# Optimization experiments

Hardware: AMD Instinct MI355X
Metric: run time of the kernel (lower is better)

## Reference

```python
import jax, jax.numpy as jnp
import numpy as np

B, T, D, L, E = 8, 2048, 256, 8, 64


def setup_inputs() -> dict:
    key = jax.random.key(0)
    ks = jax.random.split(key, 5)
    x = jax.random.normal(ks[0], (B, T, D), dtype=jnp.float32)
    # MMLP params: weight (4L, D, E), bias (4L, E); nn.Linear: (2L, D), (2L,)
    W_ml = jax.random.normal(ks[1], (4 * L, D, E), dtype=jnp.float32) * 0.05
    b_ml = jax.random.normal(ks[2], (4 * L, E), dtype=jnp.float32) * 0.05
    W_lin = jax.random.normal(ks[3], (2 * L, D), dtype=jnp.float32) * 0.05
    b_lin = jax.random.normal(ks[4], (2 * L,), dtype=jnp.float32) * 0.05
    return {"x": x, "W_ml": W_ml, "b_ml": b_ml, "W_lin": W_lin, "b_lin": b_lin}


def _xlstm_forward(x, W_ml, b_ml, W_lin, b_lin):
    b, t, _ = x.shape
    l4, _, e = W_ml.shape
    l = l4 // 4
    # Precompute all per-step gate projections at once (the torch code does this per step).
    mg = jnp.einsum('bti,lij->btlj', x, W_ml) + b_ml          # (B,T,4L,E)
    lg = jnp.einsum('bti,li->btl', x, W_lin) + b_lin          # (B,T,2L)
    o_, v, k, q = jnp.split(mg, 4, axis=2)                    # each (B,T,L,E)
    i_, f_ = jnp.split(lg, 2, axis=2)                         # each (B,T,L)
    xs = tuple(jnp.moveaxis(a, 1, 0) for a in (o_, v, k, q, i_, f_))  # time-major

    def step(carry, inp):
        m, n, C, h = carry
        o_t, v_t, k_t, q_t, i_t, f_t = inp
        m_new = jnp.maximum(f_t + m, i_t)                     # stabilizer (B,L)
        i_g = jnp.exp(i_t - m_new)
        f_g = jnp.exp(f_t + m - m_new)
        # rank-1 outer-product update of matrix cell state (B,L,E,E)
        C = f_g[:, :, None, None] * C + i_g[:, :, None, None] * (v_t[:, :, :, None] * k_t[:, :, None, :])
        n = f_g[:, :, None] * n + i_g[:, :, None] * k_t       # (B,L,E)
        denom = jnp.maximum(jnp.sum(n * q_t, axis=-1), 1.0)[:, :, None]  # clamp(.,1,inf)
        h = jax.nn.sigmoid(o_t) * jnp.einsum('blij,bli->blj', C, q_t) / denom
        return (m_new, n, C, h), None

    init = (
        jnp.zeros((b, l), jnp.float32),
        jnp.zeros((b, l, e), jnp.float32),
        jnp.zeros((b, l, e, e), jnp.float32),
        jnp.zeros((b, l, e), jnp.float32),
    )
    (m, n, C, h), _ = jax.lax.scan(step, init, xs)
    return h, C


def reference(x, W_ml, b_ml, W_lin, b_lin):
    return _xlstm_forward(x, W_ml, b_ml, W_lin, b_lin)
```

## Files before the change

### kernel.cpp

```cpp
#include <hip/hip_runtime.h>

#define B 8
#define T 2048
#define D 256
#define L 8
#define E 64
#define BT (B*T)

typedef _Float16 f16;
typedef f16 f16x8 __attribute__((ext_vector_type(8)));
typedef float f32x4 __attribute__((ext_vector_type(4)));

#define OFF_I   0
#define OFF_F   (OFF_I  + B*L*T)
#define OFF_WT  (OFF_F  + B*L*T)
#define OFF_VT  (OFF_WT + 16*E*D/2)
#define OFF_KT  (OFF_VT + B*L*E*T/2)
#define OFF_CP  (OFF_KT + B*L*E*T/2)
#define OFF_X16 (OFF_CP + 64*4*4160)

__global__ __launch_bounds__(256) void k_prep_all(const float* __restrict__ x,
        const float* __restrict__ Wlin, const float* __restrict__ blin,
        const float* __restrict__ Wml,
        float* __restrict__ ibuf, float* __restrict__ fbuf,
        f16* __restrict__ Wt16, f16* __restrict__ x16) {
    __shared__ __align__(16) char smem[49920];
    int tid = threadIdx.x;
    int bx = blockIdx.x;
    if (bx < 512) {
        float (*xs)[260] = (float(*)[260])smem;
        float (*wsm)[260] = (float(*)[260])(smem + 33280);
        int t0 = bx * 32;
        {
            int row = tid >> 3, q = tid & 7;
            const float* src = x + (size_t)(t0 + row) * D + q * 32;
            #pragma unroll
            for (int j = 0; j < 8; ++j) {
                float4 v = *(const float4*)(src + j * 4);
                *(float4*)&xs[row][q * 32 + j * 4] = v;
            }
        }
        {
            int row = tid >> 4, c0 = (tid & 15) * 16;
            const float* src = Wlin + row * D + c0;
            #pragma unroll
            for (int j = 0; j < 4; ++j) {
                float4 v = *(const float4*)(src + j * 4);
                *(float4*)&wsm[row][c0 + j * 4] = v;
            }
        }
        __syncthreads();
        int tl = tid >> 4, g = tid & 15;
        float acc0 = 0.f, acc1 = 0.f;
        for (int i = 0; i < D; ++i) {
            float wv = wsm[g][i];
            acc0 += xs[tl * 2 + 0][i] * wv;
            acc1 += xs[tl * 2 + 1][i] * wv;
        }
        float bias = blin[g];
        float acc[2] = {acc0 + bias, acc1 + bias};
        #pragma unroll
        for (int u = 0; u < 2; ++u) {
            int t = t0 + tl * 2 + u;
            int b = t >> 11, tt = t & 2047;
            if (g < 8) ibuf[(b * L + g) * T + tt] = acc[u];
            else       fbuf[(b * L + (g - 8)) * T + tt] = acc[u];
        }
    } else if (bx < 528) {
        float (*ts)[65] = (float(*)[65])smem;
        int vkrow = bx - 512;
        int wrow = 8 + vkrow;
        for (int dc = 0; dc < 4; ++dc) {
            int d0 = dc * 64;
            int r = tid >> 2, cq = (tid & 3) * 16;
            const float* src = Wml + ((size_t)wrow * D + d0 + r) * E + cq;
            #pragma unroll
            for (int j = 0; j < 16; j += 4) {
                float4 v = *(const float4*)(src + j);
                ts[r][cq + j] = v.x; ts[r][cq + j + 1] = v.y;
                ts[r][cq + j + 2] = v.z; ts[r][cq + j + 3] = v.w;
            }
            __syncthreads();
            int e = tid >> 2, dq = (tid & 3) * 16;
            f16* dst = Wt16 + ((size_t)vkrow * E + e) * D + d0 + dq;
            f16x8 o0, o1;
            #pragma unroll
            for (int j = 0; j < 8; ++j) {
                o0[j] = (f16)ts[dq + j][e];
                o1[j] = (f16)ts[dq + 8 + j][e];
            }
            *(f16x8*)dst = o0;
            *(f16x8*)(dst + 8) = o1;
            __syncthreads();
        }
    } else {
        int i = ((bx - 528) * 256 + tid) * 8;
        float4 v0 = *(const float4*)(x + i);
        float4 v1 = *(const float4*)(x + i + 4);
        f16x8 o;
        o[0] = (f16)v0.x; o[1] = (f16)v0.y; o[2] = (f16)v0.z; o[3] = (f16)v0.w;
        o[4] = (f16)v1.x; o[5] = (f16)v1.y; o[6] = (f16)v1.z; o[7] = (f16)v1.w;
        *(f16x8*)(x16 + i) = o;
    }
}

__global__ __launch_bounds__(512) void k_vkproj3(const f16* __restrict__ x16,
        const f16* __restrict__ Wt16, const float* __restrict__ bml,
        f16* __restrict__ Vt, f16* __restrict__ Kt) {
    __shared__ __align__(16) char lds[40960];
    int tid = threadIdx.x;
    int bx = blockIdx.x, h = blockIdx.y;
    int t0 = bx * 128;
    const f16* xa = x16 + (size_t)t0 * D;
    const f16* wb = Wt16 + (size_t)h * 8 * E * D;
    int wv = tid >> 6, lane = tid & 63;
    int wr = wv >> 2, wc = wv & 3;
    int q = lane >> 4, lr = lane & 15;
    int sa_t = tid >> 2, sa_q = tid & 3;
    f32x4 acc[4][8] = {};
    for (int ks = 0; ks < 8; ++ks) {
        int k0 = ks * 32;
        {
            f16x8 v = *(const f16x8*)(xa + (size_t)sa_t * D + k0 + sa_q * 8);
            int ba = sa_t * 64 + ((sa_q ^ ((sa_t >> 1) & 3)) << 4);
            *(f16x8*)(lds + ba) = v;
        }
        #pragma unroll
        for (int rr = 0; rr < 4; ++rr) {
            int r = rr * 128 + (tid >> 2);
            int c = tid & 3;
            f16x8 v = *(const f16x8*)(wb + (size_t)r * D + k0 + c * 8);
            int ba = 8192 + r * 64 + ((c ^ ((r >> 1) & 3)) << 4);
            *(f16x8*)(lds + ba) = v;
        }
        __syncthreads();
        f16x8 a[4], bf[8];
        #pragma unroll
        for (int m = 0; m < 4; ++m) {
            int t = wr * 64 + m * 16 + lr;
            int ba = t * 64 + ((q ^ ((t >> 1) & 3)) << 4);
            a[m] = *(const f16x8*)(lds + ba);
        }
        #pragma unroll
        for (int n = 0; n < 8; ++n) {
            int c = wc * 128 + n * 16 + lr;
            int ba = 8192 + c * 64 + ((q ^ ((c >> 1) & 3)) << 4);
            bf[n] = *(const f16x8*)(lds + ba);
        }
        #pragma unroll
        for (int m = 0; m < 4; ++m)
            #pragma unroll
            for (int n = 0; n < 8; ++n)
                acc[m][n] = __builtin_amdgcn_mfma_f32_16x16x32_f16(
                    a[m], bf[n], acc[m][n], 0, 0, 0);
        __syncthreads();
    }
    const float* bp = bml + (size_t)(8 + h * 8) * E;
    int b_g = t0 >> 11, tin = t0 & 2047;
    f16* obase = h ? Kt : Vt;
    for (int p = 0; p < 4; ++p) {
        if (wc == p) {
            #pragma unroll
            for (int n = 0; n < 8; ++n) {
                int cc = n * 16 + lr;
                float bias = bp[p * 128 + cc];
                int swz = (cc & 7) << 4;
                #pragma unroll
                for (int m = 0; m < 4; ++m) {
                    #pragma unroll
                    for (int r = 0; r < 4; r += 2) {
                        int t = wr * 64 + m * 16 + q * 4 + r;
                        union { f16 h2[2]; unsigned u; } pk;
                        pk.h2[0] = (f16)(acc[m][n][r] + bias);
                        pk.h2[1] = (f16)(acc[m][n][r + 1] + bias);
                        int ba = cc * 256 + ((t * 2) ^ swz);
                        *(unsigned*)(lds + ba) = pk.u;
                    }
                }
            }
        }
        __syncthreads();
        {
            int cc = tid >> 2, part = tid & 3;
            int cg = p * 128 + cc;
            int l = cg >> 6, e = cg & 63;
            f16* dst = obase + ((size_t)((b_g * L + l) * E + e)) * T + tin + part * 32;
            int swz = (cc & 7) << 4;
            #pragma unroll
            for (int jj = 0; jj < 4; ++jj) {
                int t = part * 32 + jj * 8;
                int ba = cc * 256 + ((t * 2) ^ swz);
                *(f16x8*)(dst + jj * 8) = *(const f16x8*)(lds + ba);
            }
        }
        __syncthreads();
    }
}

__global__ __launch_bounds__(256) void k_cgemm2s(const f16* __restrict__ Vt,
        const f16* __restrict__ Kt, const float* __restrict__ ibuf,
        const float* __restrict__ fbuf, float* __restrict__ Cpart) {
    __shared__ float red[64 * 64];
    __shared__ float redn[64];
    __shared__ float part[256];
    __shared__ float rmax[256];
    __shared__ __align__(16) f16 wlds[512];
    int tid = threadIdx.x;
    int bl = blockIdx.x, tc = blockIdx.y;
    int wv = tid >> 6, lane = tid & 63;
    {
        const float* fp = fbuf + bl * T + tid * 8;
        const float* ip = ibuf + bl * T + tid * 8;
        float4 fa = *(const float4*)fp;
        float4 fb = *(const float4*)(fp + 4);
        float4 ia = *(const float4*)ip;
        float4 ib = *(const float4*)(ip + 4);
        float f[8] = {fa.x, fa.y, fa.z, fa.w, fb.x, fb.y, fb.z, fb.w};
        float iv[8] = {ia.x, ia.y, ia.z, ia.w, ib.x, ib.y, ib.z, ib.w};
        float ls[8]; float run = 0.f;
        #pragma unroll
        for (int r = 0; r < 8; ++r) { run += f[r]; ls[r] = run; }
        part[tid] = run;
        __syncthreads();
        float inc = run;
        #pragma unroll
        for (int s = 1; s < 256; s <<= 1) {
            float u = (tid >= s) ? part[tid - s] : 0.f;
            __syncthreads();
            inc += u;
            part[tid] = inc;
            __syncthreads();
        }
        float off = inc - run;
        float e[8]; float lmax = -1e30f;
        #pragma unroll
        for (int r = 0; r < 8; ++r) { e[r] = iv[r] - (off + ls[r]); lmax = fmaxf(lmax, e[r]); }
        rmax[tid] = lmax;
        __syncthreads();
        for (int s = 128; s > 0; s >>= 1) {
            if (tid < s) rmax[tid] = fmaxf(rmax[tid], rmax[tid + s]);
            __syncthreads();
        }
        float M = fmaxf(rmax[0], 0.0f);
        int t = tid * 8;
        if ((t >> 9) == tc) {
            f16x8 w8;
            #pragma unroll
            for (int r = 0; r < 8; ++r) w8[r] = (f16)__expf(e[r] - M);
            *(f16x8*)&wlds[t & 511] = w8;
        }
        __syncthreads();
    }
    const f16* vp = Vt + (size_t)bl * E * T;
    const f16* kp = Kt + (size_t)bl * E * T;
    f32x4 acc[5][4] = {};
    int tbase = tc * 512 + wv * 128;
    for (int kc = 0; kc < 4; ++kc) {
        int tt = tbase + kc * 32 + (lane >> 4) * 8;
        f16x8 wfrag = *(const f16x8*)&wlds[tt & 511];
        f16x8 a[5], bf[4];
        #pragma unroll
        for (int m = 0; m < 4; ++m) {
            int i = m * 16 + (lane & 15);
            f16x8 v = *(const f16x8*)(vp + (size_t)i * T + tt);
            a[m] = v * wfrag;
        }
        a[4] = wfrag;
        #pragma unroll
        for (int nn = 0; nn < 4; ++nn) {
            int j = nn * 16 + (lane & 15);
            bf[nn] = *(const f16x8*)(kp + (size_t)j * T + tt);
        }
        #pragma unroll
        for (int m = 0; m < 5; ++m)
            #pragma unroll
            for (int nn = 0; nn < 4; ++nn)
                acc[m][nn] = __builtin_amdgcn_mfma_f32_16x16x32_f16(
                    a[m], bf[nn], acc[m][nn], 0, 0, 0);
    }
    for (int rr = 0; rr < 4; ++rr) {
        if (wv == rr) {
            #pragma unroll
            for (int m = 0; m < 4; ++m)
                #pragma unroll
                for (int nn = 0; nn < 4; ++nn)
                    #pragma unroll
                    for (int r = 0; r < 4; ++r) {
                        int row = m * 16 + (lane >> 4) * 4 + r;
                        int col = nn * 16 + (lane & 15);
                        if (rr == 0) red[row * 64 + col] = acc[m][nn][r];
                        else         red[row * 64 + col] += acc[m][nn][r];
                    }
            if ((lane >> 4) == 0) {
                #pragma unroll
                for (int nn = 0; nn < 4; ++nn) {
                    int col = nn * 16 + (lane & 15);
                    if (rr == 0) redn[col] = acc[4][nn][0];
                    else         redn[col] += acc[4][nn][0];
                }
            }
        }
        __syncthreads();
    }
    float* cp = Cpart + ((size_t)bl * 4 + tc) * 4160;
    #pragma unroll
    for (int j = 0; j < 4; ++j) {
        int idx = tid * 16 + j * 4;
        *(float4*)(cp + idx) = *(const float4*)(red + idx);
    }
    if (tid < 64) cp[4096 + tid] = redn[tid];
}

__global__ __launch_bounds__(256) void k_final(const float* __restrict__ x,
        const float* __restrict__ Wml, const float* __restrict__ bml,
        const float* __restrict__ Cpart, float* __restrict__ out) {
    __shared__ float Cs[E * E];
    __shared__ float xs[D];
    __shared__ float ns[E];
    __shared__ float os[E];
    __shared__ float qs[E];
    int tid = threadIdx.x;
    int bl = blockIdx.x; int b = bl >> 3, l = bl & 7;
    xs[tid] = x[((size_t)(b * T + (T - 1))) * D + tid];
    const float* cp = Cpart + (size_t)bl * 4 * 4160;
    #pragma unroll
    for (int j = 0; j < 4; ++j) {
        int idx = tid * 16 + j * 4;
        float4 s = {0, 0, 0, 0};
        #pragma unroll
        for (int p = 0; p < 4; ++p) {
            float4 v = *(const float4*)(cp + p * 4160 + idx);
            s.x += v.x; s.y += v.y; s.z += v.z; s.w += v.w;
        }
        *(float4*)&Cs[idx] = s;
        *(float4*)(out + 4096 + (size_t)bl * (E * E) + idx) = s;
    }
    if (tid < 64) {
        float s = 0.f;
        #pragma unroll
        for (int p = 0; p < 4; ++p) s += cp[p * 4160 + 4096 + tid];
        ns[tid] = s;
    }
    __syncthreads();
    if (tid < 128) {
        int gate = tid >> 6, e = tid & 63;
        int wrow = gate ? (3 * L + l) : l;
        const float* wpp = Wml + (size_t)wrow * D * E + e;
        float s = 0.f;
        for (int kk = 0; kk < D; ++kk) s += xs[kk] * wpp[kk * E];
        s += bml[wrow * E + e];
        if (gate) qs[e] = s; else os[e] = s;
    }
    __syncthreads();
    if (tid < 64) {
        int j = tid;
        float hc = 0.f;
        for (int i2 = 0; i2 < E; ++i2) hc += Cs[i2 * E + j] * qs[i2];
        float nq = 0.f;
        for (int i2 = 0; i2 < E; ++i2) nq += ns[i2] * qs[i2];
        float denom = fmaxf(nq, 1.0f);
        float sg = 1.0f / (1.0f + __expf(-os[j]));
        out[bl * E + j] = sg * hc / denom;
    }
}

extern "C" void kernel_launch(void* const* d_in, const int* in_sizes, int n_in,
                              void* d_out, int out_size, void* d_ws, size_t ws_size,
                              hipStream_t stream) {
    const float* x    = (const float*)d_in[0];
    const float* Wml  = (const float*)d_in[1];
    const float* bml  = (const float*)d_in[2];
    const float* Wlin = (const float*)d_in[3];
    const float* blin = (const float*)d_in[4];
    float* out = (float*)d_out;
    float* ws = (float*)d_ws;
    float* ibuf  = ws + OFF_I;
    float* fbuf  = ws + OFF_F;
    f16*   Wt16  = (f16*)(ws + OFF_WT);
    f16*   Vt    = (f16*)(ws + OFF_VT);
    f16*   Kt    = (f16*)(ws + OFF_KT);
    float* Cpart = ws + OFF_CP;
    f16*   x16   = (f16*)(ws + OFF_X16);

    k_prep_all<<<2576, 256, 0, stream>>>(x, Wlin, blin, Wml, ibuf, fbuf, Wt16, x16);
    k_vkproj3<<<dim3(BT / 128, 2), 512, 0, stream>>>(x16, Wt16, bml, Vt, Kt);
    k_cgemm2s<<<dim3(B * L, 4), 256, 0, stream>>>(Vt, Kt, ibuf, fbuf, Cpart);
    k_final<<<B * L, 256, 0, stream>>>(x, Wml, bml, Cpart, out);
}
```

Baseline: 65.34 us.

## Fuse final reduction into cgemm via atomic counter, use direct global-to-LDS loads

Measured after the change: 107.8 us. 1.65x slower.

```diff
diff --git a/kernel.cpp b/kernel.cpp
--- a/kernel.cpp
+++ b/kernel.cpp
@@ -16,14 +16,17 @@
 #define OFF_WT  (OFF_F  + B*L*T)
 #define OFF_VT  (OFF_WT + 16*E*D/2)
 #define OFF_KT  (OFF_VT + B*L*E*T/2)
-#define OFF_CP  (OFF_KT + B*L*E*T/2)
-#define OFF_X16 (OFF_CP + 64*4*4160)
-
-__global__ __launch_bounds__(256) void k_prep_all(const float* __restrict__ x,
+#define OFF_X16 (OFF_KT + B*L*E*T/2)
+#define OFF_OQ  (OFF_X16 + BT*D/2)
+#define OFF_CP  (OFF_OQ + 64*128)
+#define OFF_CNT (OFF_CP + 64*4*4160)
+
+__global__ __launch_bounds__(256) void k_prep(const float* __restrict__ x,
         const float* __restrict__ Wlin, const float* __restrict__ blin,
-        const float* __restrict__ Wml,
+        const float* __restrict__ Wml, const float* __restrict__ bml,
         float* __restrict__ ibuf, float* __restrict__ fbuf,
-        f16* __restrict__ Wt16, f16* __restrict__ x16) {
+        f16* __restrict__ Wt16, f16* __restrict__ x16,
+        float* __restrict__ oqbuf, unsigned int* __restrict__ cnt) {
     __shared__ __align__(16) char smem[49920];
     int tid = threadIdx.x;
     int bx = blockIdx.x;
@@ -93,7 +96,7 @@
             *(f16x8*)(dst + 8) = o1;
             __syncthreads();
         }
-    } else {
+    } else if (bx < 2576) {
         int i = ((bx - 528) * 256 + tid) * 8;
         float4 v0 = *(const float4*)(x + i);
         float4 v1 = *(const float4*)(x + i + 4);
@@ -101,6 +104,30 @@
         o[0] = (f16)v0.x; o[1] = (f16)v0.y; o[2] = (f16)v0.z; o[3] = (f16)v0.w;
         o[4] = (f16)v1.x; o[5] = (f16)v1.y; o[6] = (f16)v1.z; o[7] = (f16)v1.w;
         *(f16x8*)(x16 + i) = o;
+    } else if (bx < 2584) {
+        float (*x8)[256] = (float(*)[256])smem;
+        int l = bx - 2576;
+        {
+            int bb = tid >> 5, c = (tid & 31) * 8;
+            const float* src = x + ((size_t)(bb * T + (T - 1))) * D + c;
+            float4 v0 = *(const float4*)src, v1 = *(const float4*)(src + 4);
+            *(float4*)&x8[bb][c] = v0;
+            *(float4*)&x8[bb][c + 4] = v1;
+        }
+        __syncthreads();
+        #pragma unroll
+        for (int r = 0; r < 4; ++r) {
+            int idx = r * 256 + tid;
+            int gate = idx >> 9, b = (idx >> 6) & 7, e = idx & 63;
+            int row = gate ? (24 + l) : l;
+            const float* gp = Wml + (size_t)row * D * E + e;
+            float s = 0.f;
+            for (int kk = 0; kk < D; ++kk) s += x8[b][kk] * gp[(size_t)kk * E];
+            s += bml[row * E + e];
+            oqbuf[(b * L + l) * 128 + gate * 64 + e] = s;
+        }
+    } else {
+        if (tid < 64) cnt[tid] = 0u;
     }
 }
 
@@ -116,23 +143,30 @@
     int wv = tid >> 6, lane = tid & 63;
     int wr = wv >> 2, wc = wv & 3;
     int q = lane >> 4, lr = lane & 15;
-    int sa_t = tid >> 2, sa_q = tid & 3;
+    int srow_a = (wv << 4) + (lane >> 2);
+    int schk = lane & 3;
+    int sca = ((schk ^ ((srow_a >> 1) & 3)) << 3);
     f32x4 acc[4][8] = {};
     for (int ks = 0; ks < 8; ++ks) {
         int k0 = ks * 32;
         {
-            f16x8 v = *(const f16x8*)(xa + (size_t)sa_t * D + k0 + sa_q * 8);
-            int ba = sa_t * 64 + ((sa_q ^ ((sa_t >> 1) & 3)) << 4);
-            *(f16x8*)(lds + ba) = v;
+            const f16* src = xa + (size_t)srow_a * D + k0 + sca;
+            __builtin_amdgcn_global_load_lds(
+                (const __attribute__((address_space(1))) unsigned int*)src,
+                (__attribute__((address_space(3))) unsigned int*)(lds + (wv << 10)),
+                16, 0, 0);
         }
         #pragma unroll
         for (int rr = 0; rr < 4; ++rr) {
-            int r = rr * 128 + (tid >> 2);
-            int c = tid & 3;
-            f16x8 v = *(const f16x8*)(wb + (size_t)r * D + k0 + c * 8);
-            int ba = 8192 + r * 64 + ((c ^ ((r >> 1) & 3)) << 4);
-            *(f16x8*)(lds + ba) = v;
-        }
+            int r = rr * 128 + (wv << 4) + (lane >> 2);
+            int co = ((schk ^ ((r >> 1) & 3)) << 3);
+            const f16* src = wb + (size_t)r * D + k0 + co;
+            __builtin_amdgcn_global_load_lds(
+                (const __attribute__((address_space(1))) unsigned int*)src,
+                (__attribute__((address_space(3))) unsigned int*)(lds + 8192 + rr * 8192 + (wv << 10)),
+                16, 0, 0);
+        }
+        asm volatile("s_waitcnt vmcnt(0)" ::: "memory");
         __syncthreads();
         f16x8 a[4], bf[8];
         #pragma unroll
@@ -182,8 +216,8 @@
         __syncthreads();
         {
             int cc = tid >> 2, part = tid & 3;
-            int cg = p * 128 + cc;
-            int l = cg >> 6, e = cg & 63;
+            int cg2 = p * 128 + cc;
+            int l = cg2 >> 6, e = cg2 & 63;
             f16* dst = obase + ((size_t)((b_g * L + l) * E + e)) * T + tin + part * 32;
             int swz = (cc & 7) << 4;
             #pragma unroll
@@ -197,14 +231,18 @@
     }
 }
 
-__global__ __launch_bounds__(256) void k_cgemm2s(const f16* __restrict__ Vt,
+__global__ __launch_bounds__(256) void k_cgemm_fused(const f16* __restrict__ Vt,
         const f16* __restrict__ Kt, const float* __restrict__ ibuf,
-        const float* __restrict__ fbuf, float* __restrict__ Cpart) {
-    __shared__ float red[64 * 64];
-    __shared__ float redn[64];
-    __shared__ float part[256];
-    __shared__ float rmax[256];
-    __shared__ __align__(16) f16 wlds[512];
+        const float* __restrict__ fbuf, const float* __restrict__ oqbuf,
+        float* __restrict__ Cpart, unsigned int* __restrict__ cnt,
+        float* __restrict__ out) {
+    __shared__ __align__(16) char smem[18816];
+    float* red  = (float*)smem;
+    float* redn = (float*)(smem + 16384);
+    float* wtot = (float*)(smem + 16640);
+    float* wmax = (float*)(smem + 16656);
+    f16*   wlds = (f16*)(smem + 16672);
+    int*   flag = (int*)(smem + 17696);
     int tid = threadIdx.x;
     int bl = blockIdx.x, tc = blockIdx.y;
     int wv = tid >> 6, lane = tid & 63;
@@ -215,39 +253,37 @@
         float4 fb = *(const float4*)(fp + 4);
         float4 ia = *(const float4*)ip;
         float4 ib = *(const float4*)(ip + 4);
-        float f[8] = {fa.x, fa.y, fa.z, fa.w, fb.x, fb.y, fb.z, fb.w};
+        float f0[8] = {fa.x, fa.y, fa.z, fa.w, fb.x, fb.y, fb.z, fb.w};
         float iv[8] = {ia.x, ia.y, ia.z, ia.w, ib.x, ib.y, ib.z, ib.w};
         float ls[8]; float run = 0.f;
         #pragma unroll
-        for (int r = 0; r < 8; ++r) { run += f[r]; ls[r] = run; }
-        part[tid] = run;
-        __syncthreads();
-        float inc = run;
-        #pragma unroll
-        for (int s = 1; s < 256; s <<= 1) {
-            float u = (tid >= s) ? part[tid - s] : 0.f;
-            __syncthreads();
-            inc += u;
-            part[tid] = inc;
-            __syncthreads();
-        }
-        float off = inc - run;
+        for (int r = 0; r < 8; ++r) { run += f0[r]; ls[r] = run; }
+        float sc = run;
+        #pragma unroll
+        for (int s = 1; s < 64; s <<= 1) {
+            float u = __shfl_up(sc, s, 64);
+            if (lane >= s) sc += u;
+        }
+        if (lane == 63) wtot[wv] = sc;
+        __syncthreads();
+        float woff = 0.f;
+        #pragma unroll
+        for (int w2 = 0; w2 < 4; ++w2) if (w2 < wv) woff += wtot[w2];
+        float off = woff + sc - run;
         float e[8]; float lmax = -1e30f;
         #pragma unroll
         for (int r = 0; r < 8; ++r) { e[r] = iv[r] - (off + ls[r]); lmax = fmaxf(lmax, e[r]); }
-        rmax[tid] = lmax;
-        __syncthreads();
-        for (int s = 128; s > 0; s >>= 1) {
-            if (tid < s) rmax[tid] = fmaxf(rmax[tid], rmax[tid + s]);
-            __syncthreads();
-        }
-        float M = fmaxf(rmax[0], 0.0f);
-        int t = tid * 8;
-        if ((t >> 9) == tc) {
+        #pragma unroll
+        for (int s = 1; s < 64; s <<= 1) lmax = fmaxf(lmax, __shfl_xor(lmax, s, 64));
+        if (lane == 0) wmax[wv] = lmax;
+        __syncthreads();
+        float M = fmaxf(fmaxf(fmaxf(wmax[0], wmax[1]), fmaxf(wmax[2], wmax[3])), 0.f);
+        int tg = tid * 8;
+        if ((tg >> 9) == tc) {
             f16x8 w8;
             #pragma unroll
             for (int r = 0; r < 8; ++r) w8[r] = (f16)__expf(e[r] - M);
-            *(f16x8*)&wlds[t & 511] = w8;
+            *(f16x8*)&wlds[tg & 511] = w8;
         }
         __syncthreads();
     }
@@ -255,9 +291,11 @@
     const f16* kp = Kt + (size_t)bl * E * T;
     f32x4 acc[5][4] = {};
     int tbase = tc * 512 + wv * 128;
+    #pragma unroll
     for (int kc = 0; kc < 4; ++kc) {
-        int tt = tbase + kc * 32 + (lane >> 4) * 8;
-        f16x8 wfrag = *(const f16x8*)&wlds[tt & 511];
+        int lo = wv * 128 + kc * 32 + (lane >> 4) * 8;
+        int tt = tc * 512 + lo;
+        f16x8 wfrag = *(const f16x8*)&wlds[lo];
         f16x8 a[5], bf[4];
         #pragma unroll
         for (int m = 0; m < 4; ++m) {
@@ -278,6 +316,7 @@
                 acc[m][nn] = __builtin_amdgcn_mfma_f32_16x16x32_f16(
                     a[m], bf[nn], acc[m][nn], 0, 0, 0);
     }
+    (void)tbase;
     for (int rr = 0; rr < 4; ++rr) {
         if (wv == rr) {
             #pragma unroll
@@ -309,58 +348,46 @@
         *(float4*)(cp + idx) = *(const float4*)(red + idx);
     }
     if (tid < 64) cp[4096 + tid] = redn[tid];
-}
-
-__global__ __launch_bounds__(256) void k_final(const float* __restrict__ x,
-        const float* __restrict__ Wml, const float* __restrict__ bml,
-        const float* __restrict__ Cpart, float* __restrict__ out) {
-    __shared__ float Cs[E * E];
-    __shared__ float xs[D];
-    __shared__ float ns[E];
-    __shared__ float os[E];
-    __shared__ float qs[E];
-    int tid = threadIdx.x;
-    int bl = blockIdx.x; int b = bl >> 3, l = bl & 7;
-    xs[tid] = x[((size_t)(b * T + (T - 1))) * D + tid];
-    const float* cp = Cpart + (size_t)bl * 4 * 4160;
+    __threadfence();
+    if (tid == 0) {
+        unsigned old = atomicAdd(&cnt[bl], 1u);
+        *flag = (old == 3u);
+    }
+    __syncthreads();
+    if (!*flag) return;
+    __threadfence();
+    const float* cpb = Cpart + (size_t)bl * 4 * 4160;
     #pragma unroll
     for (int j = 0; j < 4; ++j) {
         int idx = tid * 16 + j * 4;
         float4 s = {0, 0, 0, 0};
         #pragma unroll
         for (int p = 0; p < 4; ++p) {
-            float4 v = *(const float4*)(cp + p * 4160 + idx);
+            float4 v = *(const float4*)(cpb + p * 4160 + idx);
             s.x += v.x; s.y += v.y; s.z += v.z; s.w += v.w;
         }
-        *(float4*)&Cs[idx] = s;
-        *(float4*)(out + 4096 + (size_t)bl * (E * E) + idx) = s;
+        *(float4*)&red[idx] = s;
+        *(float4*)(out + 4096 + (size_t)bl * 4096 + idx) = s;
     }
     if (tid < 64) {
         float s = 0.f;
         #pragma unroll
-        for (int p = 0; p < 4; ++p) s += cp[p * 4160 + 4096 + tid];
-        ns[tid] = s;
-    }
-    __syncthreads();
-    if (tid < 128) {
-        int gate = tid >> 6, e = tid & 63;
-        int wrow = gate ? (3 * L + l) : l;
-        const float* wpp = Wml + (size_t)wrow * D * E + e;
-        float s = 0.f;
-        for (int kk = 0; kk < D; ++kk) s += xs[kk] * wpp[kk * E];
-        s += bml[wrow * E + e];
-        if (gate) qs[e] = s; else os[e] = s;
+        for (int p = 0; p < 4; ++p) s += cpb[p * 4160 + 4096 + tid];
+        redn[tid] = s;
     }
     __syncthreads();
     if (tid < 64) {
         int j = tid;
-        float hc = 0.f;
-        for (int i2 = 0; i2 < E; ++i2) hc += Cs[i2 * E + j] * qs[i2];
-        float nq = 0.f;
-        for (int i2 = 0; i2 < E; ++i2) nq += ns[i2] * qs[i2];
+        float hc = 0.f, nq = 0.f;
+        const float* oq = oqbuf + bl * 128;
+        for (int i2 = 0; i2 < E; ++i2) {
+            float qv = oq[64 + i2];
+            hc += red[i2 * 64 + j] * qv;
+            nq += redn[i2] * qv;
+        }
         float denom = fmaxf(nq, 1.0f);
-        float sg = 1.0f / (1.0f + __expf(-os[j]));
-        out[bl * E + j] = sg * hc / denom;
+        float sg = 1.0f / (1.0f + __expf(-oq[j]));
+        out[bl * 64 + j] = sg * hc / denom;
     }
 }
 
@@ -379,11 +406,14 @@
     f16*   Wt16  = (f16*)(ws + OFF_WT);
     f16*   Vt    = (f16*)(ws + OFF_VT);
     f16*   Kt    = (f16*)(ws + OFF_KT);
+    f16*   x16   = (f16*)(ws + OFF_X16);
+    float* oqbuf = ws + OFF_OQ;
     float* Cpart = ws + OFF_CP;
-    f16*   x16   = (f16*)(ws + OFF_X16);
-
-    k_prep_all<<<2576, 256, 0, stream>>>(x, Wlin, blin, Wml, ibuf, fbuf, Wt16, x16);
+    unsigned int* cnt = (unsigned int*)(ws + OFF_CNT);
+
+    k_prep<<<2585, 256, 0, stream>>>(x, Wlin, blin, Wml, bml,
+                                     ibuf, fbuf, Wt16, x16, oqbuf, cnt);
     k_vkproj3<<<dim3(BT / 128, 2), 512, 0, stream>>>(x16, Wt16, bml, Vt, Kt);
-    k_cgemm2s<<<dim3(B * L, 4), 256, 0, stream>>>(Vt, Kt, ibuf, fbuf, Cpart);
-    k_final<<<B * L, 256, 0, stream>>>(x, Wml, bml, Cpart, out);
+    k_cgemm_fused<<<dim3(B * L, 4), 256, 0, stream>>>(Vt, Kt, ibuf, fbuf,
+                                                      oqbuf, Cpart, cnt, out);
 }
```
